# Performance work log

Measured on AMD Instinct MI355X. Metric: run time of the kernel, lower is better.

## Reference

```python
import jax, jax.numpy as jnp
import numpy as np
import math

DIMS, HEAD = 1024, 16
HD = DIMS // HEAD          # 64
B, CTX = 4, 1024
MAX_ITER, THRESH = 3, 0.5  # temp=1.0 -> q temperature scaling branch is skipped (as in torch)
LOG10_21 = math.log10(1.0 + 4000.0 / 200.0)


def _freq_angles(c):
    # compute_freqs_base: 0.2*(10**linspace(0, log10(21), d/2) - 1), custom_freqs = 36000/220 * base
    d2 = HD // 2
    mel = 10.0 ** jnp.linspace(0.0, LOG10_21, d2) - 1.0
    freqs = (36000.0 / 220.0) * (200.0 * mel / 1000.0)        # [d2]
    t = jnp.arange(c, dtype=jnp.float32)
    return t[:, None] * freqs[None, :]                          # [c, d2]


def _rope(x, ang):
    # lucidrains rotary_embedding_torch convention: interleaved pairs (x0,x1),(x2,x3),...
    x1, x2 = x[..., 0::2], x[..., 1::2]
    cos, sin = jnp.cos(ang), jnp.sin(ang)
    out = jnp.stack([x1 * cos - x2 * sin, x1 * sin + x2 * cos], axis=-1)
    return out.reshape(x.shape)


def _rms(x, w):
    eps = jnp.finfo(x.dtype).eps  # torch nn.RMSNorm eps=None default
    return x * jax.lax.rsqrt(jnp.mean(jnp.square(x), -1, keepdims=True) + eps) * w


def _sdpa(q, k, v):
    # mask is always None in this module's forward -> non-causal SDPA
    s = jnp.einsum('bhqd,bhkd->bhqk', q, k) / math.sqrt(q.shape[-1])
    return jnp.einsum('bhqk,bhkd->bhqd', jax.nn.softmax(s, -1), v)


def _focus(x, xa, P):
    # x: [b, cq, D] queries, xa: [b, ck, D] keys/values. In our configs cq == ck == eff_span.
    b, cq, D = x.shape
    ck = xa.shape[1]
    q = _rms(x, P['wq_norm']) @ P['Wq'] + P['bq']
    q = q.reshape(b, cq, HEAD, HD).transpose(0, 2, 1, 3)                 # b h c d
    kv = _rms(xa, P['wkv_norm']) @ P['Wkv'] + P['bkv']
    kv = kv.reshape(b, ck, 2, HEAD, HD).transpose(2, 0, 3, 1, 4)         # kv b h c d
    k, v = kv[0], kv[1]
    q = _rope(q, _freq_angles(cq))
    k = _rope(k, _freq_angles(ck))

    e = min(cq, ck)  # static; equals cq in all call sites here
    curq, kc, vc = q, k[:, :, :e], v[:, :, :e]
    prev = jnp.zeros_like(q)
    attn_out = jnp.zeros_like(q)
    done = jnp.asarray(False)
    for it in range(MAX_ITER):
        # torch: q/k/v re-projected from current state EVERY iteration (k,v compound)
        qp = curq[:, :, :e] @ P['Wlq'] + P['blq']
        kp = kc @ P['Wlk'] + P['blk']
        vp = vc @ P['Wlv'] + P['blv']
        attn = _sdpa(_rms(qp, P['wln']), _rms(kp, P['wln']), vp)         # == iter_out since e == cq
        diff = jnp.mean(jnp.abs(attn - prev))
        stop = (diff < THRESH) & (it > 0) & (~done)
        attn_out = jnp.where(done, attn_out, attn)  # on the break iteration attn_out = iter_out
        done = done | stop
        curq = jnp.where(done, curq, curq + attn)
        prev = jnp.where(done, prev, attn)
        kc = jnp.where(done, kc, kp)
        vc = jnp.where(done, vc, vp)
    return attn_out.transpose(0, 2, 1, 3).reshape(b, cq, D)             # b c (h d)


def _slide(x, P):
    # win_size = head_dim; only the first win_size keys of each span are ever used
    b, ctx, D = x.shape
    w = HD
    off = w // HEAD                       # span_len - win_size
    nwin = ctx // w                       # ctx chosen as a multiple of w
    starts = jnp.maximum(jnp.arange(nwin) * w - off, 0)
    kidx = starts[:, None] + jnp.arange(w)[None, :]                      # [nwin, w]
    qwin = x.reshape(b, nwin, w, D).transpose(1, 0, 2, 3)                # [nwin, b, w, D]
    kwin = x[:, kidx, :].transpose(1, 0, 2, 3)                           # [nwin, b, w, D]
    outw = jax.vmap(lambda xq, xk: _focus(xq, xk, P))(qwin, kwin)
    return outw.transpose(1, 0, 2, 3).reshape(b, ctx, D)


def _forward(x, xa, P):
    xw = _slide(x, P)
    xaw = _slide(xa, P)
    out = _focus(xw, xaw, P)
    return out @ P['Wo'] + P['bo']        # Dropout(0.01) is identity in eval


def setup_inputs() -> dict:
    key = jax.random.key(0)
    ks = jax.random.split(key, 8)
    s = 0.02
    f32 = jnp.float32
    return {
        'x': jax.random.normal(ks[0], (B, CTX, DIMS), f32),
        'xa': jax.random.normal(ks[1], (B, CTX, DIMS), f32),
        'wq_norm': jnp.ones((DIMS,), f32),
        'Wq': jax.random.normal(ks[2], (DIMS, DIMS), f32) * s,
        'bq': jnp.zeros((DIMS,), f32),
        'wkv_norm': jnp.ones((DIMS,), f32),
        'Wkv': jax.random.normal(ks[3], (DIMS, 2 * DIMS), f32) * s,
        'bkv': jnp.zeros((2 * DIMS,), f32),
        'wln': jnp.ones((HD,), f32),
        'Wlq': jax.random.normal(ks[4], (HD, HD), f32) * s,
        'blq': jnp.zeros((HD,), f32),
        'Wlk': jax.random.normal(ks[5], (HD, HD), f32) * s,
        'blk': jnp.zeros((HD,), f32),
        'Wlv': jax.random.normal(ks[6], (HD, HD), f32) * s,
        'blv': jnp.zeros((HD,), f32),
        'Wo': jax.random.normal(ks[7], (DIMS, DIMS), f32) * s,
        'bo': jnp.zeros((DIMS,), f32),
    }


def reference(x, xa, wq_norm, Wq, bq, wkv_norm, Wkv, bkv, wln, Wlq, blq, Wlk, blk, Wlv, blv, Wo, bo):
    P = dict(wq_norm=wq_norm, Wq=Wq, bq=bq, wkv_norm=wkv_norm, Wkv=Wkv, bkv=bkv, wln=wln,
             Wlq=Wlq, blq=blq, Wlk=Wlk, blk=blk, Wlv=Wlv, blv=blv, Wo=Wo, bo=bo)
    return _forward(x, xa, P)
```

## Files before the change

### kernel.cpp

```cpp
#include <hip/hip_runtime.h>
#include <math.h>

#define TPB 256

static __device__ __forceinline__ float4 mk4(float a, float b, float c, float d) {
  float4 r; r.x = a; r.y = b; r.z = c; r.w = d; return r;
}

static __device__ __forceinline__ float4 ld4s(const float* buf, int row, int ch) {
  return *(const float4*)&buf[(row << 6) + (((ch ^ (row >> 2)) & 15) << 2)];
}
static __device__ __forceinline__ void st4s(float* buf, int row, int ch, float4 v) {
  *(float4*)&buf[(row << 6) + (((ch ^ (row >> 2)) & 15) << 2)] = v;
}

__global__ __launch_bounds__(TPB) void k_tables(float* __restrict__ cosb,
                                                float* __restrict__ sinb) {
  int gid = blockIdx.x * TPB + threadIdx.x;
  if (gid >= 1024 * 32) return;
  int t = gid >> 5, j = gid & 31;
  const double Ld = 1.3222192947339193;
  float Lf = (float)Ld;
  float mlog;
  if (j == 31) {
    mlog = Lf;
  } else {
    float stepf = (float)((double)j / 31.0);
    mlog = (float)((double)Lf * (double)stepf);
  }
  float p = (float)pow(10.0, (double)mlog);
  float mel = p - 1.0f;
  float t2 = (200.0f * mel) / 1000.0f;
  float freq = 163.63636363636363f * t2;
  float ang = (float)t * freq;
  double a = (double)ang;
  cosb[gid] = (float)cos(a);
  sinb[gid] = (float)sin(a);
}

__global__ __launch_bounds__(TPB) void k_rowinv(const float* __restrict__ X,
                                                float* __restrict__ inv) {
  __shared__ float red[4];
  int row = blockIdx.x;
  int tid = threadIdx.x;
  float4 v = *(const float4*)(X + (size_t)row * 1024 + tid * 4);
  float ss = v.x * v.x + v.y * v.y + v.z * v.z + v.w * v.w;
#pragma unroll
  for (int m = 1; m < 64; m <<= 1) ss += __shfl_xor(ss, m);
  if ((tid & 63) == 0) red[tid >> 6] = ss;
  __syncthreads();
  if (tid == 0) {
    float s = ((red[0] + red[1]) + (red[2] + red[3]));
    float mm = s * (1.0f / 1024.0f) + 1.1920928955078125e-7f;
    inv[row] = (float)(1.0 / sqrt((double)mm));
  }
}

template <int BM, int BN>
__global__ __launch_bounds__(TPB) void k_gemm(
    const float* __restrict__ X, const float* __restrict__ inv,
    const float* __restrict__ wn, const float* __restrict__ W,
    const float* __restrict__ bias, float* __restrict__ o0,
    float* __restrict__ o1, int N, int mode) {
  constexpr int JW = BN / 64;
  constexpr int RH = BM / 64;
  constexpr int TPR = 256 / BM;
  __shared__ float As[16][BM + 4];
  int tid = threadIdx.x;
  int bx = blockIdx.x, by = blockIdx.y;
  int tx = tid & 15, ty = tid >> 4;
  float c[4 * RH][4 * JW];
#pragma unroll
  for (int i = 0; i < 4 * RH; ++i)
#pragma unroll
    for (int j = 0; j < 4 * JW; ++j) c[i][j] = 0.0f;

  int arow = tid / TPR;
  int kqb[RH];
#pragma unroll
  for (int u = 0; u < RH; ++u) kqb[u] = ((tid % TPR) * RH + u) * 4;
  float sA = 1.0f;
  if (inv) sA = inv[by * BM + arow];
  const float* Xrow = X + (size_t)(by * BM + arow) * 1024;
  const float* Wb = W + bx * BN + tx * 4;

  float4 areg[RH];
#pragma unroll
  for (int u = 0; u < RH; ++u)
    areg[u] = *(const float4*)(Xrow + kqb[u]);

  for (int k0 = 0; k0 < 1024; k0 += 16) {
#pragma unroll
    for (int u = 0; u < RH; ++u) {
      int kq = kqb[u];
      float4 a4 = areg[u];
      if (wn) {
        float4 w4 = *(const float4*)(wn + k0 + kq);
        a4.x *= w4.x; a4.y *= w4.y; a4.z *= w4.z; a4.w *= w4.w;
      }
      a4.x *= sA; a4.y *= sA; a4.z *= sA; a4.w *= sA;
      As[kq + 0][arow] = a4.x;
      As[kq + 1][arow] = a4.y;
      As[kq + 2][arow] = a4.z;
      As[kq + 3][arow] = a4.w;
    }
    __syncthreads();
    if (k0 + 16 < 1024) {
#pragma unroll
      for (int u = 0; u < RH; ++u)
        areg[u] = *(const float4*)(Xrow + k0 + 16 + kqb[u]);
    }
#pragma unroll
    for (int kk = 0; kk < 16; ++kk) {
      float av[4 * RH];
      float4 a0 = *(const float4*)&As[kk][ty * 4];
      av[0] = a0.x; av[1] = a0.y; av[2] = a0.z; av[3] = a0.w;
      if (RH == 2) {
        float4 a1 = *(const float4*)&As[kk][64 + ty * 4];
        av[4] = a1.x; av[5] = a1.y; av[6] = a1.z; av[7] = a1.w;
      }
      const float* wrow = Wb + (size_t)(k0 + kk) * N;
      float4 b0 = *(const float4*)(wrow);
      float bv[4 * JW];
      bv[0] = b0.x; bv[1] = b0.y; bv[2] = b0.z; bv[3] = b0.w;
      if (JW == 2) {
        float4 b1 = *(const float4*)(wrow + 64);
        bv[4] = b1.x; bv[5] = b1.y; bv[6] = b1.z; bv[7] = b1.w;
      }
#pragma unroll
      for (int i = 0; i < 4 * RH; ++i)
#pragma unroll
        for (int j = 0; j < 4 * JW; ++j) c[i][j] += av[i] * bv[j];
    }
    __syncthreads();
  }

#pragma unroll
  for (int jh = 0; jh < JW; ++jh) {
    int colbase = bx * BN + jh * 64 + tx * 4;
    float4 bb = {0.f, 0.f, 0.f, 0.f};
    if (bias) bb = *(const float4*)(bias + colbase);
#pragma unroll
    for (int ih = 0; ih < RH; ++ih) {
#pragma unroll
      for (int i2 = 0; i2 < 4; ++i2) {
        int row = by * BM + ih * 64 + ty * 4 + i2;
        int ci = ih * 4 + i2;
        float4 o;
        o.x = c[ci][jh * 4 + 0] + bb.x;
        o.y = c[ci][jh * 4 + 1] + bb.y;
        o.z = c[ci][jh * 4 + 2] + bb.z;
        o.w = c[ci][jh * 4 + 3] + bb.w;
        if (mode == 0) {
          *(float4*)(o0 + (size_t)row * N + colbase) = o;
        } else {
          int b = row >> 10, t = row & 1023;
          float* dst = o0;
          int cc = colbase;
          if (mode == 2 && colbase >= 1024) { dst = o1; cc = colbase - 1024; }
          int ch = cc >> 6, d = cc & 63;
          *(float4*)(dst + ((size_t)((b * 16 + ch) * 1024 + t)) * 64 + d) = o;
        }
      }
    }
  }
}

__global__ __launch_bounds__(TPB) void k_rope(float* __restrict__ A, int mask,
                                              const float* __restrict__ cosb,
                                              const float* __restrict__ sinb) {
  int gid = blockIdx.x * TPB + threadIdx.x;
  int j = gid & 31;
  int row = gid >> 5;
  int t = row & 1023;
  int aidx = ((t & mask) << 5) + j;
  float cc = cosb[aidx], sn = sinb[aidx];
  size_t base = (size_t)row * 64;
  float x1 = A[base + 2 * j], x2 = A[base + 2 * j + 1];
  A[base + 2 * j] = x1 * cc - x2 * sn;
  A[base + 2 * j + 1] = x1 * sn + x2 * cc;
}

__global__ __launch_bounds__(TPB) void k_proj(
    const float* __restrict__ curq, float* __restrict__ kc,
    float* __restrict__ vc, float* __restrict__ qph, float* __restrict__ kph,
    const float* __restrict__ Wlq, const float* __restrict__ blq,
    const float* __restrict__ Wlk, const float* __restrict__ blk,
    const float* __restrict__ Wlv, const float* __restrict__ blv,
    const float* __restrict__ wln, int CQ, const int* __restrict__ flags) {
  int RT = CQ >> 4;
  int bid = blockIdx.x;
  int rt = bid % RT;
  int rest = bid / RT;
  int h = rest & 15; rest >>= 4;
  int b = rest & 3;
  int win = rest >> 2;
  if (flags && flags[win]) return;
  __shared__ float qs[16][68], ksm[16][68], vsm[16][68];
  __shared__ float Wqs[4096], Wks[4096], Wvs[4096];
  int tid = threadIdx.x;
#pragma unroll
  for (int i = 0; i < 4; ++i) {
    int f4 = (i * 256 + tid) * 4;
    *(float4*)&Wqs[f4] = *(const float4*)(Wlq + f4);
    *(float4*)&Wks[f4] = *(const float4*)(Wlk + f4);
    *(float4*)&Wvs[f4] = *(const float4*)(Wlv + f4);
  }
  int lr = tid >> 4, c4 = (tid & 15) * 4;
  int bh = b * 16 + h;
  size_t rowbase = (size_t)bh * 1024 + (size_t)win * CQ + rt * 16;
  size_t g = (rowbase + lr) * 64 + c4;
  *(float4*)&qs[lr][c4] = *(const float4*)(curq + g);
  *(float4*)&ksm[lr][c4] = *(const float4*)(kc + g);
  *(float4*)&vsm[lr][c4] = *(const float4*)(vc + g);
  __syncthreads();
  int r = tid >> 4, cg = tid & 15;
  const float eps = 1.1920928955078125e-7f;
  float4 wl4 = *(const float4*)(wln + cg * 4);
  size_t orow = (rowbase + r) * 64 + cg * 4;
  float4 acc;
  float ssum, rms;
  acc = *(const float4*)(blq + cg * 4);
#pragma unroll 8
  for (int k = 0; k < 64; ++k) {
    float xv = qs[r][k];
    float4 w4 = *(const float4*)&Wqs[k * 64 + cg * 4];
    acc.x += xv * w4.x; acc.y += xv * w4.y;
    acc.z += xv * w4.z; acc.w += xv * w4.w;
  }
  ssum = acc.x * acc.x + acc.y * acc.y + acc.z * acc.z + acc.w * acc.w;
#pragma unroll
  for (int m = 1; m < 16; m <<= 1) ssum += __shfl_xor(ssum, m);
  rms = (float)(1.0 / sqrt((double)(ssum * 0.015625f + eps)));
  {
    float4 o;
    o.x = acc.x * rms * wl4.x; o.y = acc.y * rms * wl4.y;
    o.z = acc.z * rms * wl4.z; o.w = acc.w * rms * wl4.w;
    *(float4*)(qph + orow) = o;
  }
  acc = *(const float4*)(blk + cg * 4);
#pragma unroll 8
  for (int k = 0; k < 64; ++k) {
    float xv = ksm[r][k];
    float4 w4 = *(const float4*)&Wks[k * 64 + cg * 4];
    acc.x += xv * w4.x; acc.y += xv * w4.y;
    acc.z += xv * w4.z; acc.w += xv * w4.w;
  }
  *(float4*)(kc + orow) = acc;
  ssum = acc.x * acc.x + acc.y * acc.y + acc.z * acc.z + acc.w * acc.w;
#pragma unroll
  for (int m = 1; m < 16; m <<= 1) ssum += __shfl_xor(ssum, m);
  rms = (float)(1.0 / sqrt((double)(ssum * 0.015625f + eps)));
  {
    float4 o;
    o.x = acc.x * rms * wl4.x; o.y = acc.y * rms * wl4.y;
    o.z = acc.z * rms * wl4.z; o.w = acc.w * rms * wl4.w;
    *(float4*)(kph + orow) = o;
  }
  acc = *(const float4*)(blv + cg * 4);
#pragma unroll 8
  for (int k = 0; k < 64; ++k) {
    float xv = vsm[r][k];
    float4 w4 = *(const float4*)&Wvs[k * 64 + cg * 4];
    acc.x += xv * w4.x; acc.y += xv * w4.y;
    acc.z += xv * w4.z; acc.w += xv * w4.w;
  }
  *(float4*)(vc + orow) = acc;
}

static __device__ __forceinline__ void slide_proj_one(
    float* src, float* rawdst, float* ndst, const float* __restrict__ W,
    const float* __restrict__ bias, float4 wl4, int tx, int ty) {
  const float eps = 1.1920928955078125e-7f;
  float4 bb = *(const float4*)(bias + tx * 4);
  float4 acc[4];
#pragma unroll
  for (int i = 0; i < 4; ++i) acc[i] = bb;
#pragma unroll 2
  for (int k4 = 0; k4 < 16; ++k4) {
    const float* w = W + (k4 * 4) * 64 + tx * 4;
    float4 w0 = *(const float4*)(w);
    float4 w1 = *(const float4*)(w + 64);
    float4 w2 = *(const float4*)(w + 128);
    float4 w3 = *(const float4*)(w + 192);
#pragma unroll
    for (int i = 0; i < 4; ++i) {
      float4 a4 = ld4s(src, ty * 4 + i, k4);
      acc[i].x += a4.x * w0.x; acc[i].y += a4.x * w0.y;
      acc[i].z += a4.x * w0.z; acc[i].w += a4.x * w0.w;
      acc[i].x += a4.y * w1.x; acc[i].y += a4.y * w1.y;
      acc[i].z += a4.y * w1.z; acc[i].w += a4.y * w1.w;
      acc[i].x += a4.z * w2.x; acc[i].y += a4.z * w2.y;
      acc[i].z += a4.z * w2.z; acc[i].w += a4.z * w2.w;
      acc[i].x += a4.w * w3.x; acc[i].y += a4.w * w3.y;
      acc[i].z += a4.w * w3.z; acc[i].w += a4.w * w3.w;
    }
  }
#pragma unroll
  for (int i = 0; i < 4; ++i) {
    int row = ty * 4 + i;
    if (rawdst) st4s(rawdst, row, tx, acc[i]);
    if (ndst) {
      float ssum = acc[i].x * acc[i].x + acc[i].y * acc[i].y +
                   acc[i].z * acc[i].z + acc[i].w * acc[i].w;
#pragma unroll
      for (int mm = 1; mm < 16; mm <<= 1) ssum += __shfl_xor(ssum, mm);
      float rms = (float)(1.0 / sqrt((double)(ssum * 0.015625f + eps)));
      st4s(ndst, row, tx, mk4(acc[i].x * rms * wl4.x, acc[i].y * rms * wl4.y,
                              acc[i].z * rms * wl4.z, acc[i].w * rms * wl4.w));
    }
  }
}

__global__ __launch_bounds__(TPB) void k_slide(
    const float* __restrict__ Qg, const float* __restrict__ Kg,
    const float* __restrict__ Vg, float* __restrict__ curqg,
    float* __restrict__ kcg, float* __restrict__ vcg, float* __restrict__ outb,
    float* __restrict__ diffp, const int* __restrict__ flags,
    const float* __restrict__ cosb, const float* __restrict__ sinb,
    const float* __restrict__ Wlq, const float* __restrict__ blq,
    const float* __restrict__ Wlk, const float* __restrict__ blk,
    const float* __restrict__ Wlv, const float* __restrict__ blv,
    const float* __restrict__ wln, int mode) {
  int bid = blockIdx.x;
  int win = bid & 15, bh = bid >> 4;
  int h = bh & 15, b = bh >> 4;
  if (mode == 2 && flags[win]) return;
  __shared__ float sX[4096], sKc[4096], sVc[4096], sQp[4096], sKp[4096];
  int tid = threadIdx.x;
  int tx = tid & 15, ty = tid >> 4;
  size_t bh1024 = (size_t)bh * 1024;
  int t0 = win * 64;
  const float SCL = 0.18033688011112042f;

  if (mode == 0) {
    int sw = (win == 0) ? 0 : win * 64 - 4;
#pragma unroll
    for (int u = 0; u < 4; ++u) {
      int f4 = u * 256 + tid;
      int row = f4 >> 4, ch = f4 & 15;
      int aidx = (row << 5) + ch * 2;
      float c0 = cosb[aidx], s0 = sinb[aidx];
      float c1 = cosb[aidx + 1], s1 = sinb[aidx + 1];
      float4 q = *(const float4*)(Qg + (bh1024 + t0 + row) * 64 + ch * 4);
      st4s(sX, row, ch, mk4(q.x * c0 - q.y * s0, q.x * s0 + q.y * c0,
                            q.z * c1 - q.w * s1, q.z * s1 + q.w * c1));
      float4 k = *(const float4*)(Kg + (bh1024 + sw + row) * 64 + ch * 4);
      st4s(sKc, row, ch, mk4(k.x * c0 - k.y * s0, k.x * s0 + k.y * c0,
                             k.z * c1 - k.w * s1, k.z * s1 + k.w * c1));
      st4s(sVc, row, ch,
           *(const float4*)(Vg + (bh1024 + sw + row) * 64 + ch * 4));
    }
  } else {
#pragma unroll
    for (int u = 0; u < 4; ++u) {
      int f4 = u * 256 + tid;
      int row = f4 >> 4, ch = f4 & 15;
      size_t g = (bh1024 + t0 + row) * 64 + ch * 4;
      st4s(sX, row, ch, *(const float4*)(curqg + g));
      st4s(sKc, row, ch, *(const float4*)(kcg + g));
      st4s(sVc, row, ch, *(const float4*)(vcg + g));
    }
  }
  float4 wl4 = *(const float4*)(wln + tx * 4);
  float4 prev4[4];
  int niter = (mode == 0) ? 2 : 1;
  for (int it = 0; it < niter; ++it) {
    __syncthreads();
    slide_proj_one(sX, nullptr, sQp, Wlq, blq, wl4, tx, ty);
    slide_proj_one(sKc, sKc, sKp, Wlk, blk, wl4, tx, ty);
    slide_proj_one(sVc, sVc, nullptr, Wlv, blv, wl4, tx, ty);
    __syncthreads();
    float s4[4][4];
#pragma unroll
    for (int i = 0; i < 4; ++i)
      s4[i][0] = s4[i][1] = s4[i][2] = s4[i][3] = 0.0f;
#pragma unroll 4
    for (int d4 = 0; d4 < 16; ++d4) {
      float4 kv[4];
#pragma unroll
      for (int j = 0; j < 4; ++j) kv[j] = ld4s(sKp, tx * 4 + j, d4);
#pragma unroll
      for (int i = 0; i < 4; ++i) {
        float4 q4 = ld4s(sQp, ty * 4 + i, d4);
#pragma unroll
        for (int j = 0; j < 4; ++j) {
          s4[i][j] += q4.x * kv[j].x;
          s4[i][j] += q4.y * kv[j].y;
          s4[i][j] += q4.z * kv[j].z;
          s4[i][j] += q4.w * kv[j].w;
        }
      }
    }
    float lrow[4];
#pragma unroll
    for (int i = 0; i < 4; ++i) {
      s4[i][0] *= SCL; s4[i][1] *= SCL; s4[i][2] *= SCL; s4[i][3] *= SCL;
      float r0 = fmaxf(fmaxf(s4[i][0], s4[i][1]), fmaxf(s4[i][2], s4[i][3]));
#pragma unroll
      for (int mm = 1; mm < 16; mm <<= 1) r0 = fmaxf(r0, __shfl_xor(r0, mm));
      float rs = 0.0f;
#pragma unroll
      for (int j = 0; j < 4; ++j) {
        float pv = exp2f(s4[i][j] - r0);
        s4[i][j] = pv;
        rs += pv;
      }
#pragma unroll
      for (int mm = 1; mm < 16; mm <<= 1) rs += __shfl_xor(rs, mm);
      lrow[i] = rs;
    }
#pragma unroll
    for (int i = 0; i < 4; ++i)
      st4s(sQp, ty * 4 + i, tx, mk4(s4[i][0], s4[i][1], s4[i][2], s4[i][3]));
    float4 av[4];
#pragma unroll
    for (int i = 0; i < 4; ++i) av[i] = mk4(0.f, 0.f, 0.f, 0.f);
#pragma unroll 4
    for (int k4 = 0; k4 < 16; ++k4) {
      float4 v4[4];
#pragma unroll
      for (int kk = 0; kk < 4; ++kk) v4[kk] = ld4s(sVc, k4 * 4 + kk, tx);
#pragma unroll
      for (int i = 0; i < 4; ++i) {
        float4 p4 = ld4s(sQp, ty * 4 + i, k4);
        av[i].x += p4.x * v4[0].x; av[i].y += p4.x * v4[0].y;
        av[i].z += p4.x * v4[0].z; av[i].w += p4.x * v4[0].w;
        av[i].x += p4.y * v4[1].x; av[i].y += p4.y * v4[1].y;
        av[i].z += p4.y * v4[1].z; av[i].w += p4.y * v4[1].w;
        av[i].x += p4.z * v4[2].x; av[i].y += p4.z * v4[2].y;
        av[i].z += p4.z * v4[2].z; av[i].w += p4.z * v4[2].w;
        av[i].x += p4.w * v4[3].x; av[i].y += p4.w * v4[3].y;
        av[i].z += p4.w * v4[3].z; av[i].w += p4.w * v4[3].w;
      }
    }
#pragma unroll
    for (int i = 0; i < 4; ++i) {
      av[i].x /= lrow[i]; av[i].y /= lrow[i];
      av[i].z /= lrow[i]; av[i].w /= lrow[i];
    }
    if (mode == 0 && it == 0) {
#pragma unroll
      for (int i = 0; i < 4; ++i) {
        prev4[i] = av[i];
        int row = ty * 4 + i;
        float4 cq = ld4s(sX, row, tx);
        cq.x += av[i].x; cq.y += av[i].y; cq.z += av[i].z; cq.w += av[i].w;
        st4s(sX, row, tx, cq);
      }
    } else if (mode == 0) {
      float ds = 0.0f;
#pragma unroll
      for (int i = 0; i < 4; ++i) {
        int row = ty * 4 + i;
        ds += fabsf(av[i].x - prev4[i].x) + fabsf(av[i].y - prev4[i].y) +
              fabsf(av[i].z - prev4[i].z) + fabsf(av[i].w - prev4[i].w);
        float4 cq = ld4s(sX, row, tx);
        cq.x += av[i].x; cq.y += av[i].y; cq.z += av[i].z; cq.w += av[i].w;
        st4s(sX, row, tx, cq);
        size_t g = (bh1024 + t0 + row) * 64 + tx * 4;
        *(float4*)(curqg + g) = cq;
        *(float4*)(kcg + g) = ld4s(sKc, row, tx);
        *(float4*)(vcg + g) = ld4s(sVc, row, tx);
        size_t obase = ((size_t)b * 1024 + t0 + row) * 1024 + h * 64 + tx * 4;
        *(float4*)(outb + obase) = av[i];
      }
      __syncthreads();
      float* red = sKp;
      red[tid] = ds;
      __syncthreads();
      for (int s2 = 128; s2 > 0; s2 >>= 1) {
        if (tid < s2) red[tid] += red[tid + s2];
        __syncthreads();
      }
      if (tid == 0) diffp[bid] = red[0];
    } else {
#pragma unroll
      for (int i = 0; i < 4; ++i) {
        int row = ty * 4 + i;
        size_t obase = ((size_t)b * 1024 + t0 + row) * 1024 + h * 64 + tx * 4;
        *(float4*)(outb + obase) = av[i];
      }
    }
  }
}

__global__ __launch_bounds__(TPB) void k_attn6(
    const float* __restrict__ qph, const float* __restrict__ kph,
    const float* __restrict__ vbuf, float* __restrict__ curq,
    float* __restrict__ prevb, float* __restrict__ outb,
    float* __restrict__ diffp, const int* __restrict__ flags, int NQT, int nt,
    int mode) {
  int bid0 = blockIdx.x;
  int bid = ((bid0 & 7) << 6) | (bid0 >> 3);
  int qt = bid % NQT;
  int bh = bid / NQT;
  int h = bh & 15, b = bh >> 4;
  if (mode == 2 && flags[0]) return;
  __shared__ float sK[4096];
  __shared__ float sV[4096];
  __shared__ float sP[8192];
  int tid = threadIdx.x;
  int tx = tid & 15, ty = tid >> 4;
  size_t bh1024 = (size_t)bh * 1024;
  int q0 = qt * 128;
  const float* Qb = qph + (bh1024 + q0 + ty * 8) * 64;

  float m[8], l[8], acc[8][4];
#pragma unroll
  for (int i = 0; i < 8; ++i) {
    m[i] = -INFINITY; l[i] = 0.0f;
    acc[i][0] = acc[i][1] = acc[i][2] = acc[i][3] = 0.0f;
  }
  const float SCL = 0.18033688011112042f;

  for (int kt = 0; kt < nt; ++kt) {
    int k0 = kt * 64;
#pragma unroll
    for (int u = 0; u < 4; ++u) {
      int f4 = u * 256 + tid;
      int row = f4 >> 4, ch = f4 & 15;
      st4s(sK, row, ch,
           *(const float4*)(kph + (bh1024 + k0 + row) * 64 + ch * 4));
      st4s(sV, row, ch,
           *(const float4*)(vbuf + (bh1024 + k0 + row) * 64 + ch * 4));
    }
    __syncthreads();
    float s[8][4];
#pragma unroll
    for (int i = 0; i < 8; ++i)
      s[i][0] = s[i][1] = s[i][2] = s[i][3] = 0.0f;
#pragma unroll 4
    for (int d4 = 0; d4 < 16; ++d4) {
      float4 kv[4];
#pragma unroll
      for (int j = 0; j < 4; ++j) kv[j] = ld4s(sK, tx * 4 + j, d4);
#pragma unroll
      for (int i = 0; i < 8; ++i) {
        float4 q4 = *(const float4*)(Qb + i * 64 + d4 * 4);
#pragma unroll
        for (int j = 0; j < 4; ++j) {
          s[i][j] += q4.x * kv[j].x;
          s[i][j] += q4.y * kv[j].y;
          s[i][j] += q4.z * kv[j].z;
          s[i][j] += q4.w * kv[j].w;
        }
      }
    }
#pragma unroll
    for (int i = 0; i < 8; ++i) {
      s[i][0] *= SCL; s[i][1] *= SCL; s[i][2] *= SCL; s[i][3] *= SCL;
      float r0 = fmaxf(fmaxf(s[i][0], s[i][1]), fmaxf(s[i][2], s[i][3]));
#pragma unroll
      for (int mm = 1; mm < 16; mm <<= 1) r0 = fmaxf(r0, __shfl_xor(r0, mm));
      float mnew = fmaxf(m[i], r0);
      float sc = exp2f(m[i] - mnew);
      float rs = 0.0f;
#pragma unroll
      for (int j = 0; j < 4; ++j) {
        float pv = exp2f(s[i][j] - mnew);
        s[i][j] = pv;
        rs += pv;
      }
#pragma unroll
      for (int mm = 1; mm < 16; mm <<= 1) rs += __shfl_xor(rs, mm);
      l[i] = l[i] * sc + rs;
      m[i] = mnew;
      acc[i][0] *= sc; acc[i][1] *= sc; acc[i][2] *= sc; acc[i][3] *= sc;
    }
#pragma unroll
    for (int i = 0; i < 8; ++i) {
      int q = ty * 8 + i;
      *(float4*)&sP[(q << 6) + (((tx ^ (q >> 3)) & 15) << 2)] =
          mk4(s[i][0], s[i][1], s[i][2], s[i][3]);
    }
#pragma unroll 4
    for (int k4 = 0; k4 < 16; ++k4) {
      float4 v4[4];
#pragma unroll
      for (int kk = 0; kk < 4; ++kk) v4[kk] = ld4s(sV, k4 * 4 + kk, tx);
#pragma unroll
      for (int i = 0; i < 8; ++i) {
        int q = ty * 8 + i;
        float4 p4 = *(const float4*)&sP[(q << 6) +
                                        (((k4 ^ (q >> 3)) & 15) << 2)];
        acc[i][0] += p4.x * v4[0].x; acc[i][1] += p4.x * v4[0].y;
        acc[i][2] += p4.x * v4[0].z; acc[i][3] += p4.x * v4[0].w;
        acc[i][0] += p4.y * v4[1].x; acc[i][1] += p4.y * v4[1].y;
        acc[i][2] += p4.y * v4[1].z; acc[i][3] += p4.y * v4[1].w;
        acc[i][0] += p4.z * v4[2].x; acc[i][1] += p4.z * v4[2].y;
        acc[i][2] += p4.z * v4[2].z; acc[i][3] += p4.z * v4[2].w;
        acc[i][0] += p4.w * v4[3].x; acc[i][1] += p4.w * v4[3].y;
        acc[i][2] += p4.w * v4[3].z; acc[i][3] += p4.w * v4[3].w;
      }
    }
    __syncthreads();
  }
  float ds = 0.0f;
#pragma unroll
  for (int i = 0; i < 8; ++i) {
    int t = q0 + ty * 8 + i;
    float4 att;
    att.x = acc[i][0] / l[i];
    att.y = acc[i][1] / l[i];
    att.z = acc[i][2] / l[i];
    att.w = acc[i][3] / l[i];
    size_t base = (bh1024 + t) * 64 + tx * 4;
    size_t obase = ((size_t)b * 1024 + t) * 1024 + h * 64 + tx * 4;
    if (mode == 0) {
      *(float4*)(prevb + base) = att;
      float4 cq = *(const float4*)(curq + base);
      cq.x += att.x; cq.y += att.y; cq.z += att.z; cq.w += att.w;
      *(float4*)(curq + base) = cq;
    } else if (mode == 1) {
      float4 pv = *(const float4*)(prevb + base);
      ds += fabsf(att.x - pv.x) + fabsf(att.y - pv.y) +
            fabsf(att.z - pv.z) + fabsf(att.w - pv.w);
      float4 cq = *(const float4*)(curq + base);
      cq.x += att.x; cq.y += att.y; cq.z += att.z; cq.w += att.w;
      *(float4*)(curq + base) = cq;
      *(float4*)(outb + obase) = att;
    } else {
      *(float4*)(outb + obase) = att;
    }
  }
  if (mode == 1) {
    __syncthreads();
    float* red = sP;
    red[tid] = ds;
    __syncthreads();
    for (int s2 = 128; s2 > 0; s2 >>= 1) {
      if (tid < s2) red[tid] += red[tid + s2];
      __syncthreads();
    }
    if (tid == 0) diffp[bid] = red[0];
  }
}

__global__ __launch_bounds__(64) void k_finalize(const float* __restrict__ diffp,
                                                 int* __restrict__ flags,
                                                 int nwin, int nper,
                                                 float count) {
  int w = threadIdx.x;
  if (w < nwin) {
    float s = 0.0f;
    for (int i = 0; i < nper; ++i) s += diffp[w + i * nwin];
    flags[w] = (s / count < 0.5f) ? 1 : 0;
  }
}

extern "C" void kernel_launch(void* const* d_in, const int* in_sizes, int n_in,
                              void* d_out, int out_size, void* d_ws,
                              size_t ws_size, hipStream_t stream) {
  const float* x = (const float*)d_in[0];
  const float* xa = (const float*)d_in[1];
  const float* wqn = (const float*)d_in[2];
  const float* Wq = (const float*)d_in[3];
  const float* bq = (const float*)d_in[4];
  const float* wkvn = (const float*)d_in[5];
  const float* Wkv = (const float*)d_in[6];
  const float* bkv = (const float*)d_in[7];
  const float* wln = (const float*)d_in[8];
  const float* Wlq = (const float*)d_in[9];
  const float* blq = (const float*)d_in[10];
  const float* Wlk = (const float*)d_in[11];
  const float* blk = (const float*)d_in[12];
  const float* Wlv = (const float*)d_in[13];
  const float* blv = (const float*)d_in[14];
  const float* Wo = (const float*)d_in[15];
  const float* bo = (const float*)d_in[16];

  float* ws = (float*)d_ws;
  const size_t SLOT = (size_t)4 * 16 * 1024 * 64;
  float* xw = ws;
  float* xaw = ws + SLOT;
  float* Q = ws + 2 * SLOT;
  float* K = ws + 3 * SLOT;
  float* V = ws + 4 * SLOT;
  float* kc = ws + 5 * SLOT;
  float* vc = ws + 6 * SLOT;
  float* prev = ws + 7 * SLOT;
  float* qph = ws + 8 * SLOT;
  float* kph = ws + 9 * SLOT;
  float* misc = ws + 10 * SLOT;
  float* inv = misc;
  float* cosb = misc + 8192;
  float* sinb = cosb + 32768;
  float* diffp = sinb + 32768;
  int* flags = (int*)(diffp + 4096);

  k_tables<<<128, TPB, 0, stream>>>(cosb, sinb);

  for (int sl = 0; sl < 2; ++sl) {
    const float* Xin = sl ? xa : x;
    float* Xout = sl ? xaw : xw;
    k_rowinv<<<4096, TPB, 0, stream>>>(Xin, inv);
    k_gemm<64, 128><<<dim3(8, 64), TPB, 0, stream>>>(Xin, inv, wqn, Wq, bq, Q, nullptr, 1024, 1);
    k_gemm<128, 128><<<dim3(16, 32), TPB, 0, stream>>>(Xin, inv, wkvn, Wkv, bkv, K, V, 2048, 2);
    k_slide<<<1024, TPB, 0, stream>>>(Q, K, V, Q, kc, vc, Xout, diffp, nullptr,
                                      cosb, sinb, Wlq, blq, Wlk, blk, Wlv, blv,
                                      wln, 0);
    k_finalize<<<1, 64, 0, stream>>>(diffp, flags, 16, 64, 262144.0f);
    k_slide<<<1024, TPB, 0, stream>>>(Q, K, V, Q, kc, vc, Xout, diffp, flags,
                                      cosb, sinb, Wlq, blq, Wlk, blk, Wlv, blv,
                                      wln, 2);
  }

  k_rowinv<<<4096, TPB, 0, stream>>>(xw, inv);
  k_gemm<64, 128><<<dim3(8, 64), TPB, 0, stream>>>(xw, inv, wqn, Wq, bq, Q, nullptr, 1024, 1);
  k_rowinv<<<4096, TPB, 0, stream>>>(xaw, inv);
  k_gemm<128, 128><<<dim3(16, 32), TPB, 0, stream>>>(xaw, inv, wkvn, Wkv, bkv, K, V, 2048, 2);
  k_rope<<<8192, TPB, 0, stream>>>(Q, 1023, cosb, sinb);
  k_rope<<<8192, TPB, 0, stream>>>(K, 1023, cosb, sinb);
  float* fout = xw;
  k_proj<<<4096, TPB, 0, stream>>>(Q, K, V, qph, kph, Wlq, blq, Wlk, blk, Wlv, blv, wln, 1024, nullptr);
  k_attn6<<<512, TPB, 0, stream>>>(qph, kph, V, Q, prev, fout, diffp, nullptr, 8, 16, 0);
  k_proj<<<4096, TPB, 0, stream>>>(Q, K, V, qph, kph, Wlq, blq, Wlk, blk, Wlv, blv, wln, 1024, nullptr);
  k_attn6<<<512, TPB, 0, stream>>>(qph, kph, V, Q, prev, fout, diffp, nullptr, 8, 16, 1);
  k_finalize<<<1, 64, 0, stream>>>(diffp, flags, 1, 512, 4194304.0f);
  k_proj<<<4096, TPB, 0, stream>>>(Q, K, V, qph, kph, Wlq, blq, Wlk, blk, Wlv, blv, wln, 1024, flags);
  k_attn6<<<512, TPB, 0, stream>>>(qph, kph, V, Q, prev, fout, diffp, flags, 8, 16, 2);

  k_gemm<64, 128><<<dim3(8, 64), TPB, 0, stream>>>(fout, nullptr, nullptr, Wo, bo, (float*)d_out, nullptr, 1024, 0);
}
```

Before: 2.524 ms.

## Store normalized keys transposed and stage Q and P as outer-product tiles in attention

k_proj now writes the normalized key projection in a d-major (transposed) layout, and the attention kernel loads Q transposed into shared memory once per block. QK^T and PV then become rank-1 outer-product updates that read float4 rows from LDS, replacing per-iteration global Q reads and swizzled dot-product loads. The aim is to cut global traffic and LDS instruction count in the inner loops. In exchange, the transposed key writes in k_proj are scattered scalar stores, and two extra barriers are added per key tile.

```diff
diff --git a/kernel.cpp b/kernel.cpp
--- a/kernel.cpp
+++ b/kernel.cpp
@@ -183,7 +183,7 @@
 
 __global__ __launch_bounds__(TPB) void k_proj(
     const float* __restrict__ curq, float* __restrict__ kc,
-    float* __restrict__ vc, float* __restrict__ qph, float* __restrict__ kph,
+    float* __restrict__ vc, float* __restrict__ qph, float* __restrict__ kphT,
     const float* __restrict__ Wlq, const float* __restrict__ blq,
     const float* __restrict__ Wlk, const float* __restrict__ blk,
     const float* __restrict__ Wlv, const float* __restrict__ blv,
@@ -215,6 +215,7 @@
   *(float4*)&vsm[lr][c4] = *(const float4*)(vc + g);
   __syncthreads();
   int r = tid >> 4, cg = tid & 15;
+  int tglob = win * CQ + rt * 16 + r;
   const float eps = 1.1920928955078125e-7f;
   float4 wl4 = *(const float4*)(wln + cg * 4);
   size_t orow = (rowbase + r) * 64 + cg * 4;
@@ -252,10 +253,15 @@
   for (int m = 1; m < 16; m <<= 1) ssum += __shfl_xor(ssum, m);
   rms = (float)(1.0 / sqrt((double)(ssum * 0.015625f + eps)));
   {
-    float4 o;
-    o.x = acc.x * rms * wl4.x; o.y = acc.y * rms * wl4.y;
-    o.z = acc.z * rms * wl4.z; o.w = acc.w * rms * wl4.w;
-    *(float4*)(kph + orow) = o;
+    float no0 = acc.x * rms * wl4.x;
+    float no1 = acc.y * rms * wl4.y;
+    float no2 = acc.z * rms * wl4.z;
+    float no3 = acc.w * rms * wl4.w;
+    size_t tb = (size_t)bh * 64 + cg * 4;
+    kphT[(tb + 0) * 1024 + tglob] = no0;
+    kphT[(tb + 1) * 1024 + tglob] = no1;
+    kphT[(tb + 2) * 1024 + tglob] = no2;
+    kphT[(tb + 3) * 1024 + tglob] = no3;
   }
   acc = *(const float4*)(blv + cg * 4);
 #pragma unroll 8
@@ -485,27 +491,38 @@
   }
 }
 
-__global__ __launch_bounds__(TPB) void k_attn6(
-    const float* __restrict__ qph, const float* __restrict__ kph,
+__global__ __launch_bounds__(TPB) void k_attn9(
+    const float* __restrict__ qph, const float* __restrict__ kphT,
     const float* __restrict__ vbuf, float* __restrict__ curq,
     float* __restrict__ prevb, float* __restrict__ outb,
-    float* __restrict__ diffp, const int* __restrict__ flags, int NQT, int nt,
-    int mode) {
+    float* __restrict__ diffp, const int* __restrict__ flags, int NQT,
+    int nt, int mode) {
+  constexpr int QT = 128;
   int bid0 = blockIdx.x;
   int bid = ((bid0 & 7) << 6) | (bid0 >> 3);
   int qt = bid % NQT;
   int bh = bid / NQT;
   int h = bh & 15, b = bh >> 4;
   if (mode == 2 && flags[0]) return;
-  __shared__ float sK[4096];
-  __shared__ float sV[4096];
-  __shared__ float sP[8192];
+  __shared__ float qTs[64][QT];
+  __shared__ float kps[64 * QT];
+  __shared__ float vss[64 * 64];
   int tid = threadIdx.x;
   int tx = tid & 15, ty = tid >> 4;
   size_t bh1024 = (size_t)bh * 1024;
-  int q0 = qt * 128;
-  const float* Qb = qph + (bh1024 + q0 + ty * 8) * 64;
-
+  size_t bh64 = (size_t)bh * 64;
+  int q0 = qt * QT;
+#pragma unroll
+  for (int i = 0; i < 8; ++i) {
+    int f4id = i * 256 + tid;
+    int row = f4id >> 4;
+    int c4 = (f4id & 15) * 4;
+    float4 v = *(const float4*)(qph + (bh1024 + q0 + row) * 64 + c4);
+    qTs[c4 + 0][row] = v.x;
+    qTs[c4 + 1][row] = v.y;
+    qTs[c4 + 2][row] = v.z;
+    qTs[c4 + 3][row] = v.w;
+  }
   float m[8], l[8], acc[8][4];
 #pragma unroll
   for (int i = 0; i < 8; ++i) {
@@ -517,13 +534,14 @@
   for (int kt = 0; kt < nt; ++kt) {
     int k0 = kt * 64;
 #pragma unroll
-    for (int u = 0; u < 4; ++u) {
-      int f4 = u * 256 + tid;
-      int row = f4 >> 4, ch = f4 & 15;
-      st4s(sK, row, ch,
-           *(const float4*)(kph + (bh1024 + k0 + row) * 64 + ch * 4));
-      st4s(sV, row, ch,
-           *(const float4*)(vbuf + (bh1024 + k0 + row) * 64 + ch * 4));
+    for (int i = 0; i < 4; ++i) {
+      int f4id = i * 256 + tid;
+      int rr = f4id >> 4;
+      int c4 = (f4id & 15) * 4;
+      *(float4*)&kps[rr * QT + c4] =
+          *(const float4*)(kphT + (bh64 + rr) * 1024 + k0 + c4);
+      *(float4*)&vss[rr * 64 + c4] =
+          *(const float4*)(vbuf + (bh1024 + k0 + rr) * 64 + c4);
     }
     __syncthreads();
     float s[8][4];
@@ -531,20 +549,17 @@
     for (int i = 0; i < 8; ++i)
       s[i][0] = s[i][1] = s[i][2] = s[i][3] = 0.0f;
 #pragma unroll 4
-    for (int d4 = 0; d4 < 16; ++d4) {
-      float4 kv[4];
-#pragma unroll
-      for (int j = 0; j < 4; ++j) kv[j] = ld4s(sK, tx * 4 + j, d4);
+    for (int d = 0; d < 64; ++d) {
+      float4 kv = *(const float4*)&kps[d * QT + tx * 4];
+      float4 qa0 = *(const float4*)&qTs[d][ty * 8];
+      float4 qa1 = *(const float4*)&qTs[d][ty * 8 + 4];
+      float qv[8] = {qa0.x, qa0.y, qa0.z, qa0.w, qa1.x, qa1.y, qa1.z, qa1.w};
 #pragma unroll
       for (int i = 0; i < 8; ++i) {
-        float4 q4 = *(const float4*)(Qb + i * 64 + d4 * 4);
-#pragma unroll
-        for (int j = 0; j < 4; ++j) {
-          s[i][j] += q4.x * kv[j].x;
-          s[i][j] += q4.y * kv[j].y;
-          s[i][j] += q4.z * kv[j].z;
-          s[i][j] += q4.w * kv[j].w;
-        }
+        s[i][0] += qv[i] * kv.x;
+        s[i][1] += qv[i] * kv.y;
+        s[i][2] += qv[i] * kv.z;
+        s[i][3] += qv[i] * kv.w;
       }
     }
 #pragma unroll
@@ -568,30 +583,27 @@
       m[i] = mnew;
       acc[i][0] *= sc; acc[i][1] *= sc; acc[i][2] *= sc; acc[i][3] *= sc;
     }
-#pragma unroll
-    for (int i = 0; i < 8; ++i) {
-      int q = ty * 8 + i;
-      *(float4*)&sP[(q << 6) + (((tx ^ (q >> 3)) & 15) << 2)] =
-          mk4(s[i][0], s[i][1], s[i][2], s[i][3]);
-    }
+    __syncthreads();
+#pragma unroll
+    for (int jj = 0; jj < 4; ++jj) {
+      *(float4*)&kps[(tx * 4 + jj) * QT + ty * 8] =
+          mk4(s[0][jj], s[1][jj], s[2][jj], s[3][jj]);
+      *(float4*)&kps[(tx * 4 + jj) * QT + ty * 8 + 4] =
+          mk4(s[4][jj], s[5][jj], s[6][jj], s[7][jj]);
+    }
+    __syncthreads();
 #pragma unroll 4
-    for (int k4 = 0; k4 < 16; ++k4) {
-      float4 v4[4];
-#pragma unroll
-      for (int kk = 0; kk < 4; ++kk) v4[kk] = ld4s(sV, k4 * 4 + kk, tx);
+    for (int k = 0; k < 64; ++k) {
+      float4 vv = *(const float4*)&vss[k * 64 + tx * 4];
+      float4 pa0 = *(const float4*)&kps[k * QT + ty * 8];
+      float4 pa1 = *(const float4*)&kps[k * QT + ty * 8 + 4];
+      float pv[8] = {pa0.x, pa0.y, pa0.z, pa0.w, pa1.x, pa1.y, pa1.z, pa1.w};
 #pragma unroll
       for (int i = 0; i < 8; ++i) {
-        int q = ty * 8 + i;
-        float4 p4 = *(const float4*)&sP[(q << 6) +
-                                        (((k4 ^ (q >> 3)) & 15) << 2)];
-        acc[i][0] += p4.x * v4[0].x; acc[i][1] += p4.x * v4[0].y;
-        acc[i][2] += p4.x * v4[0].z; acc[i][3] += p4.x * v4[0].w;
-        acc[i][0] += p4.y * v4[1].x; acc[i][1] += p4.y * v4[1].y;
-        acc[i][2] += p4.y * v4[1].z; acc[i][3] += p4.y * v4[1].w;
-        acc[i][0] += p4.z * v4[2].x; acc[i][1] += p4.z * v4[2].y;
-        acc[i][2] += p4.z * v4[2].z; acc[i][3] += p4.z * v4[2].w;
-        acc[i][0] += p4.w * v4[3].x; acc[i][1] += p4.w * v4[3].y;
-        acc[i][2] += p4.w * v4[3].z; acc[i][3] += p4.w * v4[3].w;
+        acc[i][0] += pv[i] * vv.x;
+        acc[i][1] += pv[i] * vv.y;
+        acc[i][2] += pv[i] * vv.z;
+        acc[i][3] += pv[i] * vv.w;
       }
     }
     __syncthreads();
@@ -626,7 +638,7 @@
   }
   if (mode == 1) {
     __syncthreads();
-    float* red = sP;
+    float* red = vss;
     red[tid] = ds;
     __syncthreads();
     for (int s2 = 128; s2 > 0; s2 >>= 1) {
@@ -681,7 +693,7 @@
   float* vc = ws + 6 * SLOT;
   float* prev = ws + 7 * SLOT;
   float* qph = ws + 8 * SLOT;
-  float* kph = ws + 9 * SLOT;
+  float* kphT = ws + 9 * SLOT;
   float* misc = ws + 10 * SLOT;
   float* inv = misc;
   float* cosb = misc + 8192;
@@ -713,13 +725,13 @@
   k_rope<<<8192, TPB, 0, stream>>>(Q, 1023, cosb, sinb);
   k_rope<<<8192, TPB, 0, stream>>>(K, 1023, cosb, sinb);
   float* fout = xw;
-  k_proj<<<4096, TPB, 0, stream>>>(Q, K, V, qph, kph, Wlq, blq, Wlk, blk, Wlv, blv, wln, 1024, nullptr);
-  k_attn6<<<512, TPB, 0, stream>>>(qph, kph, V, Q, prev, fout, diffp, nullptr, 8, 16, 0);
-  k_proj<<<4096, TPB, 0, stream>>>(Q, K, V, qph, kph, Wlq, blq, Wlk, blk, Wlv, blv, wln, 1024, nullptr);
-  k_attn6<<<512, TPB, 0, stream>>>(qph, kph, V, Q, prev, fout, diffp, nullptr, 8, 16, 1);
+  k_proj<<<4096, TPB, 0, stream>>>(Q, K, V, qph, kphT, Wlq, blq, Wlk, blk, Wlv, blv, wln, 1024, nullptr);
+  k_attn9<<<512, TPB, 0, stream>>>(qph, kphT, V, Q, prev, fout, diffp, nullptr, 8, 16, 0);
+  k_proj<<<4096, TPB, 0, stream>>>(Q, K, V, qph, kphT, Wlq, blq, Wlk, blk, Wlv, blv, wln, 1024, nullptr);
+  k_attn9<<<512, TPB, 0, stream>>>(qph, kphT, V, Q, prev, fout, diffp, nullptr, 8, 16, 1);
   k_finalize<<<1, 64, 0, stream>>>(diffp, flags, 1, 512, 4194304.0f);
-  k_proj<<<4096, TPB, 0, stream>>>(Q, K, V, qph, kph, Wlq, blq, Wlk, blk, Wlv, blv, wln, 1024, flags);
-  k_attn6<<<512, TPB, 0, stream>>>(qph, kph, V, Q, prev, fout, diffp, flags, 8, 16, 2);
+  k_proj<<<4096, TPB, 0, stream>>>(Q, K, V, qph, kphT, Wlq, blq, Wlk, blk, Wlv, blv, wln, 1024, flags);
+  k_attn9<<<512, TPB, 0, stream>>>(qph, kphT, V, Q, prev, fout, diffp, flags, 8, 16, 2);
 
   k_gemm<64, 128><<<dim3(8, 64), TPB, 0, stream>>>(fout, nullptr, nullptr, Wo, bo, (float*)d_out, nullptr, 1024, 0);
 }
```

New measurement: 2.402 ms. 1.05x faster.
